# Kernel tuning notes

Measured on AMD Instinct MI355X. Metric: run time of the kernel, lower is better.

Reference implementation:

```python
import jax, jax.numpy as jnp
import numpy as np


def setup_inputs() -> dict:
    key = jax.random.key(0)
    x = jax.random.normal(key, (16, 2048, 512), dtype=jnp.float32)
    return {"x": x}


def reference(x):
    # Cosine (L2-normalized) self-attention.
    # norm: [B, N, 1] L2 norm over feature dim
    norm = jnp.sqrt(jnp.sum(x * x, axis=2, keepdims=True))
    # scores[b, i, j] = <x_i, x_j> / (|x_i| |x_j|)  -> [B, N, N]
    scores = jnp.einsum('bnd,bmd->bnm', x, x) / (norm * jnp.swapaxes(norm, -2, -1))
    p_attn = jax.nn.softmax(scores, axis=-1)
    # output: [B, N, D]
    return jnp.einsum('bnm,bmd->bnd', p_attn, x)
```

## Files before the change

kernel.cpp:

```cpp
#include <hip/hip_runtime.h>
#include <hip/hip_bf16.h>
#include <cstdint>
#include <cstddef>

#define BB 16
#define NN 2048
#define DD 512

typedef _Float16 f16x8 __attribute__((ext_vector_type(8)));
typedef _Float16 f16x4 __attribute__((ext_vector_type(4)));
typedef float f32x4 __attribute__((ext_vector_type(4)));
typedef unsigned int u32x4 __attribute__((ext_vector_type(4)));

__device__ __forceinline__ void async_ld16(void* lds, const void* g) {
    __builtin_amdgcn_global_load_lds(
        (const __attribute__((address_space(1))) unsigned int*)(uintptr_t)g,
        (__attribute__((address_space(3))) unsigned int*)(uint32_t)(uintptr_t)lds,
        16, 0, 0);
}

#define VM_WAIT(n) asm volatile("s_waitcnt vmcnt(" #n ")" ::: "memory")
#define RAW_BAR()  do { asm volatile("" ::: "memory"); __builtin_amdgcn_s_barrier(); asm volatile("" ::: "memory"); } while (0)
#define LGKM_BAR() do { asm volatile("s_waitcnt lgkmcnt(0)" ::: "memory"); \
                        __builtin_amdgcn_s_barrier();                      \
                        __builtin_amdgcn_sched_barrier(0); } while (0)

__global__ __launch_bounds__(256) void k_prep(const float* __restrict__ x,
                                              _Float16* __restrict__ xhn,
                                              _Float16* __restrict__ vT,
                                              float* __restrict__ denom) {
    __shared__ _Float16 t[512 * 66];
    const int tid = threadIdx.x, lane = tid & 63, w = tid >> 6;
    const int b = blockIdx.y, j0 = blockIdx.x * 64;
    if (tid < 64) denom[b * NN + j0 + tid] = 0.f;
    const float* xb = x + ((size_t)b * NN + j0) * DD;

    for (int rr = 0; rr < 16; ++rr) {
        const int jj = w * 16 + rr;
        const float* xr = xb + (size_t)jj * DD;
        f32x4 a = __builtin_nontemporal_load((const f32x4*)xr + lane);
        f32x4 c = __builtin_nontemporal_load((const f32x4*)xr + lane + 64);
        float ss = a[0]*a[0] + a[1]*a[1] + a[2]*a[2] + a[3]*a[3]
                 + c[0]*c[0] + c[1]*c[1] + c[2]*c[2] + c[3]*c[3];
        #pragma unroll
        for (int o = 1; o < 64; o <<= 1) ss += __shfl_xor(ss, o);
        const float rn = 1.0f / sqrtf(ss);
        _Float16* dst = xhn + ((size_t)b * NN + j0 + jj) * DD;
        f16x4 v0 = {(_Float16)(a[0]*rn), (_Float16)(a[1]*rn), (_Float16)(a[2]*rn), (_Float16)(a[3]*rn)};
        f16x4 v1 = {(_Float16)(c[0]*rn), (_Float16)(c[1]*rn), (_Float16)(c[2]*rn), (_Float16)(c[3]*rn)};
        *(f16x4*)(dst + 4 * lane) = v0;
        *(f16x4*)(dst + 256 + 4 * lane) = v1;
        const int d0 = 4 * lane, d1 = 256 + 4 * lane;
        t[(d0 + 0) * 66 + jj] = (_Float16)a[0];
        t[(d0 + 1) * 66 + jj] = (_Float16)a[1];
        t[(d0 + 2) * 66 + jj] = (_Float16)a[2];
        t[(d0 + 3) * 66 + jj] = (_Float16)a[3];
        t[(d1 + 0) * 66 + jj] = (_Float16)c[0];
        t[(d1 + 1) * 66 + jj] = (_Float16)c[1];
        t[(d1 + 2) * 66 + jj] = (_Float16)c[2];
        t[(d1 + 3) * 66 + jj] = (_Float16)c[3];
    }
    LGKM_BAR();
    #pragma unroll
    for (int it = 0; it < 16; ++it) {
        const int id = it * 256 + tid;
        const int d = id >> 3, ch = (id & 7) * 8;
        const uint32_t* tp = (const uint32_t*)&t[d * 66 + ch];
        uint4 v = {tp[0], tp[1], tp[2], tp[3]};
        *(uint4*)(vT + ((size_t)b * DD + d) * NN + j0 + ch) = v;
    }
}

__global__ __launch_bounds__(256, 4) void k_scores(const _Float16* __restrict__ xhn,
                                                   _Float16* __restrict__ W,
                                                   float* __restrict__ denom) {
    __shared__ _Float16 smem[17408];
    const int tid = threadIdx.x;
    const int lane = tid & 63, wv = tid >> 6;
    const int wr = wv >> 1, wc = wv & 1;
    const int m_ = lane & 15, quad = lane >> 4;
    const int b = blockIdx.z;

    const int swz = (blockIdx.x % 8) * 17 + blockIdx.x / 8;
    int rem = swz, ti = 0, rowlen = NN / 128;
    while (rem >= rowlen) { rem -= rowlen; ++ti; --rowlen; }
    const int tj = ti + rem;
    const int I = ti * 128, J = tj * 128;
    const bool diag = (ti == tj);

    const _Float16* Ab = xhn + ((size_t)b * NN + I) * DD;
    const _Float16* Bb = xhn + ((size_t)b * NN + J) * DD;

    f32x4 acc[4][4];
    #pragma unroll
    for (int i = 0; i < 4; ++i)
        #pragma unroll
        for (int j = 0; j < 4; ++j) acc[i][j] = (f32x4){0.f, 0.f, 0.f, 0.f};

    const int srw = lane >> 2;
    const int sck = lane & 3;
    const int soff = ((sck ^ ((srw >> 1) & 3)) * 8);
    const _Float16* agl = Ab + (size_t)(wv * 16 + srw) * DD + soff;
    const _Float16* bgl = Bb + (size_t)(wv * 16 + srw) * DD + soff;

#define S_STG(kb_) do {                                                       \
    _Float16* A_ = smem + (((kb_) & 1) << 13);   \
    const int k0_ = (kb_) * 32;                                               \
    async_ld16(&A_[(wv * 16) * 32],             agl + k0_);                   \
    async_ld16(&A_[(64 + wv * 16) * 32],        agl + (size_t)64 * DD + k0_); \
    async_ld16(&A_[4096 + (wv * 16) * 32],      bgl + k0_);                   \
    async_ld16(&A_[4096 + (64 + wv * 16) * 32], bgl + (size_t)64 * DD + k0_); \
    } while (0)

    S_STG(0); S_STG(1);
    for (int kb = 0; kb < DD / 32; ++kb) {
        if (kb == DD / 32 - 1) { VM_WAIT(0); } else { VM_WAIT(4); }
        RAW_BAR();
        const _Float16* As_ = smem + ((kb & 1) << 13);
        const _Float16* Bs_ = As_ + 4096;
        __builtin_amdgcn_s_setprio(1);
        {
            f16x8 af[4], bf[4];
            #pragma unroll
            for (int t = 0; t < 4; ++t) {
                const int Ra = wr * 64 + t * 16 + m_;
                const int Rb = wc * 64 + t * 16 + m_;
                af[t] = *(const f16x8*)&As_[Ra * 32 + ((quad ^ ((Ra >> 1) & 3)) * 8)];
                bf[t] = *(const f16x8*)&Bs_[Rb * 32 + ((quad ^ ((Rb >> 1) & 3)) * 8)];
            }
            #pragma unroll
            for (int i = 0; i < 4; ++i)
                #pragma unroll
                for (int j = 0; j < 4; ++j)
                    acc[i][j] = __builtin_amdgcn_mfma_f32_16x16x32_f16(af[i], bf[j], acc[i][j], 0, 0, 0);
        }
        __builtin_amdgcn_s_setprio(0);
        RAW_BAR();
        if (kb + 2 < DD / 32) S_STG(kb + 2);
    }
#undef S_STG

    f16x4 wq[4][4];
    float rowpart[4][4];
    float colpart[4] = {0.f, 0.f, 0.f, 0.f};
    #pragma unroll
    for (int i = 0; i < 4; ++i)
        #pragma unroll
        for (int r = 0; r < 4; ++r) rowpart[i][r] = 0.f;

    #pragma unroll
    for (int i = 0; i < 4; ++i) {
        #pragma unroll
        for (int j = 0; j < 4; ++j) {
            #pragma unroll
            for (int r = 0; r < 4; ++r) {
                const float w = __expf(acc[i][j][r]);
                wq[i][j][r] = (_Float16)w;
                rowpart[i][r] += w;
                colpart[j] += w;
            }
        }
    }

    _Float16* WtT = smem;
    #pragma unroll
    for (int i = 0; i < 4; ++i) {
        const int rowb = wr * 64 + i * 16 + quad * 4;
        #pragma unroll
        for (int j = 0; j < 4; ++j) {
            const int col = wc * 64 + j * 16 + m_;
            *(f16x4*)&WtT[col * 136 + rowb] = wq[i][j];
        }
    }
    LGKM_BAR();
    #pragma unroll
    for (int it2 = 0; it2 < 8; ++it2) {
        const int id = it2 * 256 + tid;
        const int rr = id >> 4, off = (id & 15) * 8;
        *(uint4*)(W + ((size_t)b * NN + J + rr) * NN + I + off) =
            *(const uint4*)&WtT[rr * 136 + off];
    }

    #pragma unroll
    for (int i = 0; i < 4; ++i) {
        #pragma unroll
        for (int r = 0; r < 4; ++r) {
            float s = rowpart[i][r];
            s += __shfl_xor(s, 1);
            s += __shfl_xor(s, 2);
            s += __shfl_xor(s, 4);
            s += __shfl_xor(s, 8);
            if (m_ == 0)
                atomicAdd(&denom[b * NN + I + wr * 64 + i * 16 + quad * 4 + r], s);
        }
    }
    if (!diag) {
        #pragma unroll
        for (int j = 0; j < 4; ++j) {
            float s = colpart[j];
            s += __shfl_xor(s, 16);
            s += __shfl_xor(s, 32);
            if (quad == 0)
                atomicAdd(&denom[b * NN + J + wc * 64 + j * 16 + m_], s);
        }
    }

    if (!diag) {
        LGKM_BAR();
        _Float16* Wt = smem;
        #pragma unroll
        for (int i = 0; i < 4; ++i) {
            const int rowb = wr * 64 + i * 16 + quad * 4;
            #pragma unroll
            for (int j = 0; j < 4; ++j) {
                const int col = wc * 64 + j * 16 + m_;
                #pragma unroll
                for (int r = 0; r < 4; ++r)
                    Wt[(rowb + r) * 136 + col] = wq[i][j][r];
            }
        }
        LGKM_BAR();
        #pragma unroll
        for (int it2 = 0; it2 < 8; ++it2) {
            const int id = it2 * 256 + tid;
            const int rr = id >> 4, off = (id & 15) * 8;
            *(uint4*)(W + ((size_t)b * NN + I + rr) * NN + J + off) =
                *(const uint4*)&Wt[rr * 136 + off];
        }
    }
}

__global__ __launch_bounds__(256, 4) void k_pv(const _Float16* __restrict__ W,
                                               const _Float16* __restrict__ vT,
                                               const float* __restrict__ denom,
                                               float* __restrict__ out) {
    __shared__ _Float16 As[8192];
    __shared__ _Float16 Bs[8192];
    __shared__ float rdI[128];
    const int tid = threadIdx.x;
    const int lane = tid & 63, w = tid >> 6;
    const int wr = w >> 1, wc = w & 1;
    const int m_ = lane & 15, quad = lane >> 4;

    const int bx = blockIdx.x;
    const int xcd = bx & 7, slot = bx >> 3;
    const int b  = (slot >> 6) * 8 + xcd;
    const int r_ = slot & 63;
    const int I  = (r_ >> 2) * 128;
    const int D0 = (r_ & 3) * 128;

    float dv = 0.f;
    if (tid < 128) dv = denom[b * NN + I + tid];

    const _Float16* Ab = W  + ((size_t)b * NN + I) * NN;
    const _Float16* Bb = vT + ((size_t)b * DD + D0) * NN;

    const int sub = lane >> 3;
    const int swc = (lane & 7) ^ sub;
    const _Float16* agl = Ab + (size_t)(w * 32 + sub) * NN + swc * 8;
    const _Float16* bgl = Bb + (size_t)(w * 32 + sub) * NN + swc * 8;

    f32x4 acc[4][4];
    #pragma unroll
    for (int i = 0; i < 4; ++i)
        #pragma unroll
        for (int j = 0; j < 4; ++j) acc[i][j] = (f32x4){0.f, 0.f, 0.f, 0.f};

    for (int kb = 0; kb < NN / 64; ++kb) {
        const int k0 = kb * 64;
        #pragma unroll
        for (int c = 0; c < 4; ++c) {
            async_ld16(&As[(w * 32 + c * 8) * 64], agl + (size_t)c * 8 * NN + k0);
            async_ld16(&Bs[(w * 32 + c * 8) * 64], bgl + (size_t)c * 8 * NN + k0);
        }
        VM_WAIT(0);
        RAW_BAR();
        __builtin_amdgcn_s_setprio(1);
        #pragma unroll
        for (int kc = 0; kc < 2; ++kc) {
            f16x8 af[4], bf[4];
            #pragma unroll
            for (int t = 0; t < 4; ++t) {
                const int Ra = wr * 64 + t * 16 + m_;
                const int Rb = wc * 64 + t * 16 + m_;
                af[t] = *(const f16x8*)&As[Ra * 64 + (((kc * 4 + quad) ^ (Ra & 7)) * 8)];
                bf[t] = *(const f16x8*)&Bs[Rb * 64 + (((kc * 4 + quad) ^ (Rb & 7)) * 8)];
            }
            #pragma unroll
            for (int i = 0; i < 4; ++i)
                #pragma unroll
                for (int j = 0; j < 4; ++j)
                    acc[i][j] = __builtin_amdgcn_mfma_f32_16x16x32_f16(af[i], bf[j], acc[i][j], 0, 0, 0);
        }
        __builtin_amdgcn_s_setprio(0);
        RAW_BAR();
    }

    if (tid < 128) rdI[tid] = 1.0f / dv;
    LGKM_BAR();

    #pragma unroll
    for (int i = 0; i < 4; ++i) {
        const int rowb = wr * 64 + i * 16 + quad * 4;
        #pragma unroll
        for (int r = 0; r < 4; ++r) {
            const float sc = rdI[rowb + r];
            float* op = out + ((size_t)(b * NN + I + rowb + r)) * DD + D0;
            #pragma unroll
            for (int j = 0; j < 4; ++j)
                __builtin_nontemporal_store(acc[i][j][r] * sc,
                                            op + wc * 64 + j * 16 + m_);
        }
    }
}

extern "C" void kernel_launch(void* const* d_in, const int* in_sizes, int n_in,
                              void* d_out, int out_size, void* d_ws, size_t ws_size,
                              hipStream_t stream) {
    const float* x = (const float*)d_in[0];
    char* ws = (char*)d_ws;
    _Float16* xhn   = (_Float16*)(ws);
    _Float16* vT    = (_Float16*)(ws + (size_t)33554432);
    _Float16* W     = (_Float16*)(ws + (size_t)67108864);
    float*    denom = (float*)   (ws + (size_t)201326592);
    float*    out   = (float*)d_out;

    k_prep<<<dim3(NN / 64, BB), 256, 0, stream>>>(x, xhn, vT, denom);
    const int npairs = (NN / 128) * (NN / 128 + 1) / 2;
    k_scores<<<dim3(npairs, 1, BB), 256, 0, stream>>>(xhn, W, denom);
    k_pv<<<dim3(1024, 1, 1), 256, 0, stream>>>(W, vT, denom, out);
}
```

Measured before the change: 170.2 us.

## Double-buffer PV kernel LDS loads with 32-wide K tiles and prefetch

The PV GEMM kernel previously loaded a 64-wide K tile, waited for all loads, computed, and then loaded the next tile. It now uses two 32-wide K-tile buffers in the same LDS footprint, prefetching tile kb+2 while tile kb is computed, with a partial vmcnt wait. A new XOR swizzle is used for the 32-element rows. This aims to hide global load latency behind the MFMAs, at the cost of more iterations and twice as many barriers per unit of K.

Result: slower. 179.0 us (+5.2%).

```diff
diff --git a/kernel.cpp b/kernel.cpp
--- a/kernel.cpp
+++ b/kernel.cpp
@@ -234,8 +234,7 @@
                                                const _Float16* __restrict__ vT,
                                                const float* __restrict__ denom,
                                                float* __restrict__ out) {
-    __shared__ _Float16 As[8192];
-    __shared__ _Float16 Bs[8192];
+    __shared__ _Float16 smem[16384];
     __shared__ float rdI[128];
     const int tid = threadIdx.x;
     const int lane = tid & 63, w = tid >> 6;
@@ -255,10 +254,11 @@
     const _Float16* Ab = W  + ((size_t)b * NN + I) * NN;
     const _Float16* Bb = vT + ((size_t)b * DD + D0) * NN;
 
-    const int sub = lane >> 3;
-    const int swc = (lane & 7) ^ sub;
-    const _Float16* agl = Ab + (size_t)(w * 32 + sub) * NN + swc * 8;
-    const _Float16* bgl = Bb + (size_t)(w * 32 + sub) * NN + swc * 8;
+    const int srw = lane >> 2;
+    const int sck = lane & 3;
+    const int soff = ((sck ^ ((srw >> 1) & 3)) * 8);
+    const _Float16* agl = Ab + (size_t)(w * 16 + srw) * NN + soff;
+    const _Float16* bgl = Bb + (size_t)(w * 16 + srw) * NN + soff;
 
     f32x4 acc[4][4];
     #pragma unroll
@@ -266,25 +266,30 @@
         #pragma unroll
         for (int j = 0; j < 4; ++j) acc[i][j] = (f32x4){0.f, 0.f, 0.f, 0.f};
 
-    for (int kb = 0; kb < NN / 64; ++kb) {
-        const int k0 = kb * 64;
-        #pragma unroll
-        for (int c = 0; c < 4; ++c) {
-            async_ld16(&As[(w * 32 + c * 8) * 64], agl + (size_t)c * 8 * NN + k0);
-            async_ld16(&Bs[(w * 32 + c * 8) * 64], bgl + (size_t)c * 8 * NN + k0);
-        }
-        VM_WAIT(0);
+#define P_STG(kb_) do {                                                       \
+    _Float16* A_ = smem + (((kb_) & 1) << 13);   \
+    const int k0_ = (kb_) * 32;                                               \
+    async_ld16(&A_[(w * 16) * 32],             agl + k0_);                    \
+    async_ld16(&A_[(64 + w * 16) * 32],        agl + (size_t)64 * NN + k0_);  \
+    async_ld16(&A_[4096 + (w * 16) * 32],      bgl + k0_);                    \
+    async_ld16(&A_[4096 + (64 + w * 16) * 32], bgl + (size_t)64 * NN + k0_);  \
+    } while (0)
+
+    P_STG(0); P_STG(1);
+    for (int kb = 0; kb < NN / 32; ++kb) {
+        if (kb == NN / 32 - 1) { VM_WAIT(0); } else { VM_WAIT(4); }
         RAW_BAR();
+        const _Float16* As_ = smem + ((kb & 1) << 13);
+        const _Float16* Bs_ = As_ + 4096;
         __builtin_amdgcn_s_setprio(1);
-        #pragma unroll
-        for (int kc = 0; kc < 2; ++kc) {
+        {
             f16x8 af[4], bf[4];
             #pragma unroll
             for (int t = 0; t < 4; ++t) {
                 const int Ra = wr * 64 + t * 16 + m_;
                 const int Rb = wc * 64 + t * 16 + m_;
-                af[t] = *(const f16x8*)&As[Ra * 64 + (((kc * 4 + quad) ^ (Ra & 7)) * 8)];
-                bf[t] = *(const f16x8*)&Bs[Rb * 64 + (((kc * 4 + quad) ^ (Rb & 7)) * 8)];
+                af[t] = *(const f16x8*)&As_[Ra * 32 + ((quad ^ ((Ra >> 1) & 3)) * 8)];
+                bf[t] = *(const f16x8*)&Bs_[Rb * 32 + ((quad ^ ((Rb >> 1) & 3)) * 8)];
             }
             #pragma unroll
             for (int i = 0; i < 4; ++i)
@@ -294,7 +299,9 @@
         }
         __builtin_amdgcn_s_setprio(0);
         RAW_BAR();
-    }
+        if (kb + 2 < NN / 32) P_STG(kb + 2);
+    }
+#undef P_STG
 
     if (tid < 128) rdI[tid] = 1.0f / dv;
     LGKM_BAR();
```
